# Kernel optimization log

Hardware: AMD Instinct MI355X
Metric: run time of the kernel (lower is better)

Reference implementation:

```python
import jax, jax.numpy as jnp
import numpy as np

DIM = 768
HEADS = 12
HEAD_DIM = DIM // HEADS
SCALE = HEAD_DIM ** -0.5


def setup_inputs() -> dict:
    key = jax.random.key(0)
    ks = jax.random.split(key, 6)
    B, N, M, C = 4, 2048, 1024, DIM
    x = jax.random.normal(ks[0], (B, N, C), dtype=jnp.float32)
    r = jax.random.normal(ks[1], (B, M, C), dtype=jnp.float32)
    s = 1.0 / np.sqrt(C)
    W_q = jax.random.normal(ks[2], (C, C), dtype=jnp.float32) * s
    W_kv = jax.random.normal(ks[3], (C, 2 * C), dtype=jnp.float32) * s
    W_proj = jax.random.normal(ks[4], (C, C), dtype=jnp.float32) * s
    b_proj = jax.random.normal(ks[5], (C,), dtype=jnp.float32) * 0.02
    return {"x": x, "r": r, "W_q": W_q, "W_kv": W_kv, "W_proj": W_proj, "b_proj": b_proj}


def reference(x, r, W_q, W_kv, W_proj, b_proj):
    B, N, C = x.shape
    _, M, _ = r.shape
    H, D = HEADS, C // HEADS
    # projections (no bias on q/kv per qkv_bias=False)
    q = (x @ W_q).reshape(B, N, H, D)            # bnhd
    kv = (r @ W_kv).reshape(B, M, 2, H, D)
    k = kv[:, :, 0]                               # bmhd
    v = kv[:, :, 1]                               # bmhd
    attn = jnp.einsum('bnhd,bmhd->bhnm', q, k) * SCALE
    attn = jax.nn.softmax(attn, axis=-1)
    out = jnp.einsum('bhnm,bmhd->bnhd', attn, v).reshape(B, N, C)
    return out @ W_proj + b_proj
```

## Files before the change

### kernel.cpp

```cpp
#include <hip/hip_runtime.h>
#include <hip/hip_bf16.h>
#include <cstdint>

#define HEADS 12

typedef __attribute__((ext_vector_type(8))) __bf16 bf16x8;
typedef __attribute__((ext_vector_type(4))) __bf16 bf16x4;
typedef __attribute__((ext_vector_type(4))) float f32x4;
typedef __attribute__((ext_vector_type(16))) float f32x16;

#define AS1 __attribute__((address_space(1)))
#define AS3 __attribute__((address_space(3)))

__device__ __forceinline__ void gload16(const void* src, void* lds) {
  __builtin_amdgcn_global_load_lds((AS1 void*)src, (AS3 void*)lds, 16, 0, 0);
}

__device__ __forceinline__ uint32_t cvtpk(float lo, float hi) {
  uint32_t r;
  asm("v_cvt_pk_bf16_f32 %0, %1, %2" : "=v"(r) : "v"(lo), "v"(hi));
  return r;
}

__device__ __forceinline__ float exp2_fast(float x) {
  float r;
  asm("v_exp_f32 %0, %1" : "=v"(r) : "v"(x));
  return r;
}

__global__ void k_prep(const float* __restrict__ x, const float* __restrict__ r,
                       const float* __restrict__ Wq, const float* __restrict__ Wkv,
                       const float* __restrict__ Wp,
                       __bf16* __restrict__ xb, __bf16* __restrict__ rb,
                       __bf16* __restrict__ wqt, __bf16* __restrict__ wkvt,
                       __bf16* __restrict__ wpt) {
  __shared__ float tile[32][33];
  const int bid = blockIdx.x, tid = threadIdx.x;
  if (bid < 9216) {
    int i = (bid * 256 + tid) * 4;
    const float* src;
    __bf16* dst;
    int off;
    if (i < 6291456) { src = x; dst = xb; off = i; }
    else             { src = r; dst = rb; off = i - 6291456; }
    float4 v = *(const float4*)(src + off);
    bf16x4 o;
    o[0] = (__bf16)v.x; o[1] = (__bf16)v.y; o[2] = (__bf16)v.z; o[3] = (__bf16)v.w;
    *(bf16x4*)(dst + off) = o;
    return;
  }
  int wb = bid - 9216;
  int z = wb / 1152, rem = wb % 1152;
  int nt = rem % 48, kt = rem / 48;
  const float* W; __bf16* Wt; int N; float scale;
  if (z == 0)      { W = Wq;  Wt = wqt;  N = 768;  scale = 0.18033688011112042f; }
  else if (z == 1) { W = Wkv; Wt = wkvt; N = 1536; scale = 1.0f; }
  else             { W = Wp;  Wt = wpt;  N = 768;  scale = 1.0f; }
  if (nt * 32 >= N) return;
  int c = tid & 31, r0 = tid >> 5;
#pragma unroll
  for (int i = 0; i < 4; ++i) {
    int rr = r0 + i * 8;
    tile[rr][c] = W[(size_t)(kt * 32 + rr) * N + nt * 32 + c];
  }
  __syncthreads();
#pragma unroll
  for (int i = 0; i < 4; ++i) {
    int rr = r0 + i * 8;
    Wt[(size_t)(nt * 32 + rr) * 768 + kt * 32 + c] = (__bf16)(tile[c][rr] * scale);
  }
}

__global__ __launch_bounds__(256, 4) void k_gemm12(
    const __bf16* __restrict__ xb, const __bf16* __restrict__ rb,
    const __bf16* __restrict__ wqt, const __bf16* __restrict__ wkvt,
    __bf16* __restrict__ qb, __bf16* __restrict__ kbp, __bf16* __restrict__ vbp) {
  __shared__ __align__(16) char lds[4][8192];
  const int tid = threadIdx.x;
  const int ln = tid & 63;
  const int w = tid >> 6;
  int id = blockIdx.x;
  id = (id & 7) * 96 + (id >> 3);
  const __bf16* A; const __bf16* Bt; int bm0, bn0; bool qpart;
  if (id < 384) { A = xb; Bt = wqt;  bm0 = (id / 6) * 128;  bn0 = (id % 6) * 128;  qpart = true; }
  else { int i2 = id - 384; A = rb; Bt = wkvt; bm0 = (i2 / 12) * 128; bn0 = (i2 % 12) * 128; qpart = false; }
  const int wm0 = (w >> 1) * 64, wn0 = (w & 1) * 64;

  auto stage = [&](char* buf, const __bf16* G, int row0, int k0) {
    const char* gb = (const char*)(G + (size_t)row0 * 768 + k0);
#pragma unroll
    for (int c = 0; c < 2; ++c) {
      int off = c * 4096 + tid * 16;
      int row = off >> 6;
      int s = ((off >> 4) & 3) ^ ((row >> 1) & 3);
      gload16(gb + (size_t)row * 1536 + (s << 4), buf + c * 4096 + (w << 10));
    }
  };

  f32x4 acc[4][4] = {};
  stage(lds[0], A, bm0, 0);
  stage(lds[2], Bt, bn0, 0);
  __syncthreads();
  for (int kt = 0; kt < 24; ++kt) {
    const char* bufA = lds[kt & 1];
    const char* bufB = lds[2 + (kt & 1)];
    if (kt + 1 < 24) {
      stage(lds[(kt + 1) & 1], A, bm0, (kt + 1) * 32);
      stage(lds[2 + ((kt + 1) & 1)], Bt, bn0, (kt + 1) * 32);
    }
    bf16x8 af[4], bf[4];
#pragma unroll
    for (int mt = 0; mt < 4; ++mt) {
      int row = wm0 + mt * 16 + (ln & 15);
      af[mt] = *(const bf16x8*)(bufA + row * 64 + ((((ln >> 4)) ^ ((row >> 1) & 3)) << 4));
    }
#pragma unroll
    for (int nt = 0; nt < 4; ++nt) {
      int row = wn0 + nt * 16 + (ln & 15);
      bf[nt] = *(const bf16x8*)(bufB + row * 64 + ((((ln >> 4)) ^ ((row >> 1) & 3)) << 4));
    }
    __builtin_amdgcn_s_setprio(1);
#pragma unroll
    for (int mt = 0; mt < 4; ++mt)
#pragma unroll
      for (int nt = 0; nt < 4; ++nt)
        acc[mt][nt] = __builtin_amdgcn_mfma_f32_16x16x32_bf16(af[mt], bf[nt], acc[mt][nt], 0, 0, 0);
    __builtin_amdgcn_s_setprio(0);
    __syncthreads();
  }

  char* ldsT = &lds[0][0];
  const bool vpart = (!qpart) && (bn0 >= 768);
  if (!vpart) {
#pragma unroll
    for (int mt = 0; mt < 4; ++mt)
#pragma unroll
      for (int nt = 0; nt < 4; ++nt)
#pragma unroll
        for (int jj = 0; jj < 4; ++jj) {
          int rowl = wm0 + mt * 16 + ((ln >> 4) << 2) + jj;
          int colb = (wn0 + nt * 16 + (ln & 15)) * 2;
          *(__bf16*)(ldsT + rowl * 256 + (colb ^ ((rowl & 7) << 4))) = (__bf16)acc[mt][nt][jj];
        }
  } else {
#pragma unroll
    for (int mt = 0; mt < 4; ++mt)
#pragma unroll
      for (int nt = 0; nt < 4; ++nt)
#pragma unroll
        for (int jj = 0; jj < 4; ++jj) {
          int dloc = wn0 + nt * 16 + (ln & 15);
          int kvb = (wm0 + mt * 16 + ((ln >> 4) << 2) + jj) * 2;
          *(__bf16*)(ldsT + dloc * 256 + (kvb ^ ((dloc & 7) << 4))) = (__bf16)acc[mt][nt][jj];
        }
  }
  __syncthreads();

  if (qpart) {
#pragma unroll
    for (int it = 0; it < 8; ++it) {
      int rowl = it * 16 + (tid >> 4);
      int colb = (tid & 15) * 16;
      bf16x8 v = *(const bf16x8*)(ldsT + rowl * 256 + (colb ^ ((rowl & 7) << 4)));
      *(bf16x8*)(qb + (size_t)(bm0 + rowl) * 768 + bn0 + (tid & 15) * 8) = v;
    }
  } else if (!vpart) {
    const int bb = bm0 >> 10, kvb0 = (bm0 & 1023) >> 5, hh0 = bn0 >> 6;
#pragma unroll
    for (int it = 0; it < 8; ++it) {
      int hh = it >> 2, t32 = it & 3;
      int dc = tid >> 5, kvl = tid & 31;
      int rowl = t32 * 32 + kvl;
      int colb = hh * 128 + (dc >> 1) * 32 + (dc & 1) * 16;
      bf16x8 v = *(const bf16x8*)(ldsT + rowl * 256 + (colb ^ ((rowl & 7) << 4)));
      *(bf16x8*)(kbp + ((size_t)(bb * 12 + hh0 + hh) * 32 + kvb0 + t32) * 2048 + tid * 8) = v;
    }
  } else {
    const int bb = bm0 >> 10, kvb0 = (bm0 & 1023) >> 5, hh0 = (bn0 - 768) >> 6;
#pragma unroll
    for (int it = 0; it < 8; ++it) {
      int hh = it >> 2, t32 = it & 3;
      int d = ((tid >> 7) << 5) + (tid & 31);
      int kvl8 = (((tid >> 6) & 1) << 4) + (((tid >> 5) & 1) << 3);
      int dloc = hh * 64 + d;
      int kvb = (t32 * 32 + kvl8) * 2;
      bf16x8 v = *(const bf16x8*)(ldsT + dloc * 256 + (kvb ^ ((dloc & 7) << 4)));
      *(bf16x8*)(vbp + ((size_t)(bb * 12 + hh0 + hh) * 32 + kvb0 + t32) * 2048 + tid * 8) = v;
    }
  }
}

__global__ __launch_bounds__(256, 4) void k_gemmP(
    const __bf16* __restrict__ A, const __bf16* __restrict__ Bt,
    float* __restrict__ C, const float* __restrict__ bias) {
  __shared__ __align__(16) char lds[4][8192];
  const int tid = threadIdx.x;
  const int ln = tid & 63;
  const int w = tid >> 6;
  int bid = blockIdx.y * 6 + blockIdx.x;
  bid = (bid & 7) * 48 + (bid >> 3);
  const int bm0 = (bid / 6) * 128, bn0 = (bid % 6) * 128;
  const int wm0 = (w >> 1) * 64, wn0 = (w & 1) * 64;

  auto stage = [&](char* buf, const __bf16* G, int row0, int k0) {
    const char* gb = (const char*)(G + (size_t)row0 * 768 + k0);
#pragma unroll
    for (int c = 0; c < 2; ++c) {
      int off = c * 4096 + tid * 16;
      int row = off >> 6;
      int s = ((off >> 4) & 3) ^ ((row >> 1) & 3);
      gload16(gb + (size_t)row * 1536 + (s << 4), buf + c * 4096 + (w << 10));
    }
  };

  f32x4 acc[4][4] = {};
  stage(lds[0], A, bm0, 0);
  stage(lds[2], Bt, bn0, 0);
  __syncthreads();
  for (int kt = 0; kt < 24; ++kt) {
    const char* bufA = lds[kt & 1];
    const char* bufB = lds[2 + (kt & 1)];
    if (kt + 1 < 24) {
      stage(lds[(kt + 1) & 1], A, bm0, (kt + 1) * 32);
      stage(lds[2 + ((kt + 1) & 1)], Bt, bn0, (kt + 1) * 32);
    }
    bf16x8 af[4], bf[4];
#pragma unroll
    for (int mt = 0; mt < 4; ++mt) {
      int row = wm0 + mt * 16 + (ln & 15);
      af[mt] = *(const bf16x8*)(bufA + row * 64 + ((((ln >> 4)) ^ ((row >> 1) & 3)) << 4));
    }
#pragma unroll
    for (int nt = 0; nt < 4; ++nt) {
      int row = wn0 + nt * 16 + (ln & 15);
      bf[nt] = *(const bf16x8*)(bufB + row * 64 + ((((ln >> 4)) ^ ((row >> 1) & 3)) << 4));
    }
    __builtin_amdgcn_s_setprio(1);
#pragma unroll
    for (int mt = 0; mt < 4; ++mt)
#pragma unroll
      for (int nt = 0; nt < 4; ++nt)
        acc[mt][nt] = __builtin_amdgcn_mfma_f32_16x16x32_bf16(af[mt], bf[nt], acc[mt][nt], 0, 0, 0);
    __builtin_amdgcn_s_setprio(0);
    __syncthreads();
  }
#pragma unroll
  for (int mt = 0; mt < 4; ++mt) {
    int row = bm0 + wm0 + mt * 16 + ((ln >> 4) << 2);
#pragma unroll
    for (int nt = 0; nt < 4; ++nt) {
      int col = bn0 + wn0 + nt * 16 + (ln & 15);
      float bv = bias[col];
#pragma unroll
      for (int jj = 0; jj < 4; ++jj)
        C[(size_t)(row + jj) * 768 + col] = acc[mt][nt][jj] + bv;
    }
  }
}

__global__ __launch_bounds__(256, 3) void k_attn(
    const __bf16* __restrict__ q, const __bf16* __restrict__ kb,
    const __bf16* __restrict__ vb, __bf16* __restrict__ ao) {
  __shared__ __align__(16) char ldsK[3][16384];
  const int tid = threadIdx.x, ln = tid & 63;
  const int l5 = ln >> 5, l32 = ln & 31, w = tid >> 6;
  int id = blockIdx.y * 16 + blockIdx.x;
  id = (id & 7) * 96 + (id >> 3);
  const int qt = id & 15, bh = id >> 4;
  const int b = bh / HEADS, h = bh % HEADS;
  const int qrow = b * 2048 + qt * 128 + w * 32 + l32;

  const char* kbase = (const char*)kb + (size_t)bh * 131072;
  const __bf16* vbase = vb + (size_t)bh * 65536;
  const int vchunk = l5 * 256 + l32 * 8;

  auto stageKpair = [&](int p, int buf) {
#pragma unroll
    for (int c = 0; c < 4; ++c)
      gload16(kbase + (size_t)p * 16384 + c * 4096 + tid * 16, ldsK[buf] + c * 4096 + tid * 16);
  };

  bf16x8 qf[4];
#pragma unroll
  for (int s = 0; s < 4; ++s)
    qf[s] = *(const bf16x8*)(q + (size_t)qrow * 768 + h * 64 + 16 * s + 8 * l5);

  stageKpair(0, 0);
  stageKpair(1, 1);

  f32x16 accO[2] = {};
  f32x4 lp = {0.f, 0.f, 0.f, 0.f};

  asm volatile("s_waitcnt vmcnt(0)" ::: "memory");
  __builtin_amdgcn_s_barrier();

  for (int p = 0; p < 8; ++p) {
    const char* bufK = ldsK[p % 3];
    if (p < 6) stageKpair(p + 2, (p + 2) % 3);

#pragma unroll
    for (int sub = 0; sub < 2; ++sub) {
      const int t = 2 * p + sub;
      const char* bK = bufK + sub * 8192;

      bf16x8 vf[2][2][2];
      {
        const __bf16* vt = vbase + (size_t)(2 * t) * 2048 + vchunk;
#pragma unroll
        for (int nt = 0; nt < 2; ++nt)
#pragma unroll
          for (int dt = 0; dt < 2; ++dt)
#pragma unroll
            for (int ks = 0; ks < 2; ++ks)
              vf[nt][dt][ks] = *(const bf16x8*)(vt + nt * 2048 + (dt * 2 + ks) * 512);
      }

      f32x16 s16[2] = {};
      __builtin_amdgcn_s_setprio(1);
#pragma unroll
      for (int s = 0; s < 4; ++s) {
        bf16x8 kf0 = *(const bf16x8*)(bK + (s * 2 + l5) * 512 + l32 * 16);
        s16[0] = __builtin_amdgcn_mfma_f32_32x32x16_bf16(kf0, qf[s], s16[0], 0, 0, 0);
        bf16x8 kf1 = *(const bf16x8*)(bK + 4096 + (s * 2 + l5) * 512 + l32 * 16);
        s16[1] = __builtin_amdgcn_mfma_f32_32x32x16_bf16(kf1, qf[s], s16[1], 0, 0, 0);
      }
      __builtin_amdgcn_s_setprio(0);

#pragma unroll
      for (int nt = 0; nt < 2; ++nt)
#pragma unroll
        for (int i = 0; i < 16; ++i) {
          float e = exp2_fast(s16[nt][i]);
          s16[nt][i] = e;
          lp[i & 3] += e;
        }

      bf16x8 pk[2][2];
#pragma unroll
      for (int nt = 0; nt < 2; ++nt) {
        uint32_t c0[4], c1[4];
#pragma unroll
        for (int j = 0; j < 4; ++j) {
          c0[j] = cvtpk(s16[nt][4 * j], s16[nt][4 * j + 1]);
          c1[j] = cvtpk(s16[nt][4 * j + 2], s16[nt][4 * j + 3]);
        }
        uint32_t w00 = c0[0], w02 = c0[1];
        asm("v_permlane32_swap_b32 %0, %1" : "+v"(w00), "+v"(w02));
        uint32_t w01 = c1[0], w03 = c1[1];
        asm("v_permlane32_swap_b32 %0, %1" : "+v"(w01), "+v"(w03));
        uint32_t w10 = c0[2], w12 = c0[3];
        asm("v_permlane32_swap_b32 %0, %1" : "+v"(w10), "+v"(w12));
        uint32_t w11 = c1[2], w13 = c1[3];
        asm("v_permlane32_swap_b32 %0, %1" : "+v"(w11), "+v"(w13));
        union { uint32_t u[4]; bf16x8 v; } pk0, pk1;
        pk0.u[0] = w00; pk0.u[1] = w01; pk0.u[2] = w02; pk0.u[3] = w03;
        pk1.u[0] = w10; pk1.u[1] = w11; pk1.u[2] = w12; pk1.u[3] = w13;
        pk[nt][0] = pk0.v;
        pk[nt][1] = pk1.v;
      }

      __builtin_amdgcn_s_setprio(1);
#pragma unroll
      for (int nt = 0; nt < 2; ++nt)
#pragma unroll
        for (int ks = 0; ks < 2; ++ks) {
          accO[0] = __builtin_amdgcn_mfma_f32_32x32x16_bf16(vf[nt][0][ks], pk[nt][ks], accO[0], 0, 0, 0);
          accO[1] = __builtin_amdgcn_mfma_f32_32x32x16_bf16(vf[nt][1][ks], pk[nt][ks], accO[1], 0, 0, 0);
        }
      __builtin_amdgcn_s_setprio(0);
    }

    __builtin_amdgcn_sched_barrier(0);
    __builtin_amdgcn_s_barrier();
  }

  float lrow = (lp[0] + lp[1]) + (lp[2] + lp[3]);
  float l = lrow + __shfl_xor(lrow, 32, 64);
  float inv = 1.0f / l;
  size_t rowb = (size_t)qrow * 768 + h * 64;
#pragma unroll
  for (int dt = 0; dt < 2; ++dt)
#pragma unroll
    for (int j = 0; j < 4; ++j) {
      bf16x4 o;
#pragma unroll
      for (int i = 0; i < 4; ++i) o[i] = (__bf16)(accO[dt][4 * j + i] * inv);
      *(bf16x4*)(ao + rowb + dt * 32 + 8 * j + 4 * l5) = o;
    }
}

extern "C" void kernel_launch(void* const* d_in, const int* in_sizes, int n_in,
                              void* d_out, int out_size, void* d_ws, size_t ws_size,
                              hipStream_t stream) {
  const float* x = (const float*)d_in[0];
  const float* r = (const float*)d_in[1];
  const float* Wq = (const float*)d_in[2];
  const float* Wkv = (const float*)d_in[3];
  const float* Wp = (const float*)d_in[4];
  const float* bp = (const float*)d_in[5];

  char* ws = (char*)d_ws;
  __bf16* xb  = (__bf16*)ws; ws += (size_t)6291456 * 2;
  __bf16* rb  = (__bf16*)ws; ws += (size_t)3145728 * 2;
  __bf16* wqt = (__bf16*)ws; ws += (size_t)589824 * 2;
  __bf16* wkvt= (__bf16*)ws; ws += (size_t)1179648 * 2;
  __bf16* wpt = (__bf16*)ws; ws += (size_t)589824 * 2;
  __bf16* qb  = (__bf16*)ws; ws += (size_t)6291456 * 2;
  __bf16* kbk = (__bf16*)ws; ws += (size_t)3145728 * 2;
  __bf16* vbk = (__bf16*)ws; ws += (size_t)3145728 * 2;
  __bf16* ao  = (__bf16*)ws;

  k_prep<<<12672, 256, 0, stream>>>(x, r, Wq, Wkv, Wp, xb, rb, wqt, wkvt, wpt);
  k_gemm12<<<768, 256, 0, stream>>>(xb, rb, wqt, wkvt, qb, kbk, vbk);
  k_attn<<<dim3(16, 48), 256, 0, stream>>>(qb, kbk, vbk, ao);
  k_gemmP<<<dim3(6, 64), 256, 0, stream>>>(ao, wpt, (float*)d_out, bp);
}
```

Baseline: 96.42 us.

## Triple-buffer GEMM K-loop staging and prefetch both V tiles per attention step

Both projection GEMM kernels move from double to triple LDS buffering. Loads are staged two k-steps ahead, and the full __syncthreads is replaced by a partial vmcnt wait plus a barrier, so global loads stay in flight across iterations. The attention kernel now issues the V-fragment loads for both sub-tiles at the start of each outer step, before the K staging, so their latency overlaps more compute. The costs are more LDS per block, which lowers the occupancy bound from 4 to 3, and more live registers in attention.

Measured after the change: 100.3 us. +4.0%, slower.

```diff
diff --git a/kernel.cpp b/kernel.cpp
--- a/kernel.cpp
+++ b/kernel.cpp
@@ -71,11 +71,11 @@
   }
 }
 
-__global__ __launch_bounds__(256, 4) void k_gemm12(
+__global__ __launch_bounds__(256, 3) void k_gemm12(
     const __bf16* __restrict__ xb, const __bf16* __restrict__ rb,
     const __bf16* __restrict__ wqt, const __bf16* __restrict__ wkvt,
     __bf16* __restrict__ qb, __bf16* __restrict__ kbp, __bf16* __restrict__ vbp) {
-  __shared__ __align__(16) char lds[4][8192];
+  __shared__ __align__(16) char lds[6][8192];
   const int tid = threadIdx.x;
   const int ln = tid & 63;
   const int w = tid >> 6;
@@ -99,14 +99,18 @@
 
   f32x4 acc[4][4] = {};
   stage(lds[0], A, bm0, 0);
-  stage(lds[2], Bt, bn0, 0);
-  __syncthreads();
+  stage(lds[3], Bt, bn0, 0);
+  stage(lds[1], A, bm0, 32);
+  stage(lds[4], Bt, bn0, 32);
+  asm volatile("s_waitcnt vmcnt(4)" ::: "memory");
+  __builtin_amdgcn_s_barrier();
+
   for (int kt = 0; kt < 24; ++kt) {
-    const char* bufA = lds[kt & 1];
-    const char* bufB = lds[2 + (kt & 1)];
-    if (kt + 1 < 24) {
-      stage(lds[(kt + 1) & 1], A, bm0, (kt + 1) * 32);
-      stage(lds[2 + ((kt + 1) & 1)], Bt, bn0, (kt + 1) * 32);
+    const char* bufA = lds[kt % 3];
+    const char* bufB = lds[3 + kt % 3];
+    if (kt + 2 < 24) {
+      stage(lds[(kt + 2) % 3], A, bm0, (kt + 2) * 32);
+      stage(lds[3 + (kt + 2) % 3], Bt, bn0, (kt + 2) * 32);
     }
     bf16x8 af[4], bf[4];
 #pragma unroll
@@ -126,8 +130,15 @@
       for (int nt = 0; nt < 4; ++nt)
         acc[mt][nt] = __builtin_amdgcn_mfma_f32_16x16x32_bf16(af[mt], bf[nt], acc[mt][nt], 0, 0, 0);
     __builtin_amdgcn_s_setprio(0);
-    __syncthreads();
-  }
+    __builtin_amdgcn_sched_barrier(0);
+    if (kt < 22) {
+      asm volatile("s_waitcnt vmcnt(4)" ::: "memory");
+    } else {
+      asm volatile("s_waitcnt vmcnt(0)" ::: "memory");
+    }
+    __builtin_amdgcn_s_barrier();
+  }
+  __syncthreads();
 
   char* ldsT = &lds[0][0];
   const bool vpart = (!qpart) && (bn0 >= 768);
@@ -190,10 +201,10 @@
   }
 }
 
-__global__ __launch_bounds__(256, 4) void k_gemmP(
+__global__ __launch_bounds__(256, 3) void k_gemmP(
     const __bf16* __restrict__ A, const __bf16* __restrict__ Bt,
     float* __restrict__ C, const float* __restrict__ bias) {
-  __shared__ __align__(16) char lds[4][8192];
+  __shared__ __align__(16) char lds[6][8192];
   const int tid = threadIdx.x;
   const int ln = tid & 63;
   const int w = tid >> 6;
@@ -215,14 +226,18 @@
 
   f32x4 acc[4][4] = {};
   stage(lds[0], A, bm0, 0);
-  stage(lds[2], Bt, bn0, 0);
-  __syncthreads();
+  stage(lds[3], Bt, bn0, 0);
+  stage(lds[1], A, bm0, 32);
+  stage(lds[4], Bt, bn0, 32);
+  asm volatile("s_waitcnt vmcnt(4)" ::: "memory");
+  __builtin_amdgcn_s_barrier();
+
   for (int kt = 0; kt < 24; ++kt) {
-    const char* bufA = lds[kt & 1];
-    const char* bufB = lds[2 + (kt & 1)];
-    if (kt + 1 < 24) {
-      stage(lds[(kt + 1) & 1], A, bm0, (kt + 1) * 32);
-      stage(lds[2 + ((kt + 1) & 1)], Bt, bn0, (kt + 1) * 32);
+    const char* bufA = lds[kt % 3];
+    const char* bufB = lds[3 + kt % 3];
+    if (kt + 2 < 24) {
+      stage(lds[(kt + 2) % 3], A, bm0, (kt + 2) * 32);
+      stage(lds[3 + (kt + 2) % 3], Bt, bn0, (kt + 2) * 32);
     }
     bf16x8 af[4], bf[4];
 #pragma unroll
@@ -242,7 +257,13 @@
       for (int nt = 0; nt < 4; ++nt)
         acc[mt][nt] = __builtin_amdgcn_mfma_f32_16x16x32_bf16(af[mt], bf[nt], acc[mt][nt], 0, 0, 0);
     __builtin_amdgcn_s_setprio(0);
-    __syncthreads();
+    __builtin_amdgcn_sched_barrier(0);
+    if (kt < 22) {
+      asm volatile("s_waitcnt vmcnt(4)" ::: "memory");
+    } else {
+      asm volatile("s_waitcnt vmcnt(0)" ::: "memory");
+    }
+    __builtin_amdgcn_s_barrier();
   }
 #pragma unroll
   for (int mt = 0; mt < 4; ++mt) {
@@ -296,25 +317,24 @@
 
   for (int p = 0; p < 8; ++p) {
     const char* bufK = ldsK[p % 3];
+
+    bf16x8 vfA[2][2][2], vfB[2][2][2];
+    {
+      const __bf16* vt0 = vbase + (size_t)(4 * p) * 2048 + vchunk;
+      const __bf16* vt1 = vbase + (size_t)(4 * p + 2) * 2048 + vchunk;
+#pragma unroll
+      for (int nt = 0; nt < 2; ++nt)
+#pragma unroll
+        for (int dt = 0; dt < 2; ++dt)
+#pragma unroll
+          for (int ks = 0; ks < 2; ++ks) {
+            vfA[nt][dt][ks] = *(const bf16x8*)(vt0 + nt * 2048 + (dt * 2 + ks) * 512);
+            vfB[nt][dt][ks] = *(const bf16x8*)(vt1 + nt * 2048 + (dt * 2 + ks) * 512);
+          }
+    }
     if (p < 6) stageKpair(p + 2, (p + 2) % 3);
 
-#pragma unroll
-    for (int sub = 0; sub < 2; ++sub) {
-      const int t = 2 * p + sub;
-      const char* bK = bufK + sub * 8192;
-
-      bf16x8 vf[2][2][2];
-      {
-        const __bf16* vt = vbase + (size_t)(2 * t) * 2048 + vchunk;
-#pragma unroll
-        for (int nt = 0; nt < 2; ++nt)
-#pragma unroll
-          for (int dt = 0; dt < 2; ++dt)
-#pragma unroll
-            for (int ks = 0; ks < 2; ++ks)
-              vf[nt][dt][ks] = *(const bf16x8*)(vt + nt * 2048 + (dt * 2 + ks) * 512);
-      }
-
+    auto SUB = [&](const char* bK, bf16x8 (&vf)[2][2][2]) {
       f32x16 s16[2] = {};
       __builtin_amdgcn_s_setprio(1);
 #pragma unroll
@@ -368,7 +388,10 @@
           accO[1] = __builtin_amdgcn_mfma_f32_32x32x16_bf16(vf[nt][1][ks], pk[nt][ks], accO[1], 0, 0, 0);
         }
       __builtin_amdgcn_s_setprio(0);
-    }
+    };
+
+    SUB(bufK, vfA);
+    SUB(bufK + 8192, vfB);
 
     __builtin_amdgcn_sched_barrier(0);
     __builtin_amdgcn_s_barrier();
```
